# Kernel tuning notes

Measured on AMD Instinct MI355X. Metric: run time of the kernel, lower is better.

The kernel has to match this reference:

```python
import jax, jax.numpy as jnp
import numpy as np

N_NODES = 100000
N_EDGES = 1600000
D_IN = 128
D_OUT = 128


def setup_inputs() -> dict:
    key = jax.random.key(0)
    k1, k2, k3, k4, k5 = jax.random.split(key, 5)
    h = jax.random.normal(k1, (N_NODES, D_IN), dtype=jnp.float32)
    src = jax.random.randint(k2, (N_EDGES,), 0, N_NODES, dtype=jnp.int64)
    dst = jax.random.randint(k3, (N_EDGES,), 0, N_NODES, dtype=jnp.int64)
    # Glorot-ish init for linear weights (PyTorch nn.Linear style: [out, in])
    scale = 1.0 / np.sqrt(D_IN)
    W_self = jax.random.uniform(k4, (D_OUT, D_IN), jnp.float32, -scale, scale)
    W_neigh = jax.random.uniform(k5, (D_OUT, D_IN), jnp.float32, -scale, scale)
    b = jnp.zeros((D_OUT,), dtype=jnp.float32)
    return {"h": h, "src": src, "dst": dst, "W_self": W_self,
            "W_neigh": W_neigh, "b": b}


def reference(h, src, dst, W_self, W_neigh, b):
    n_nodes = h.shape[0]
    # neighbor gather + segment-mean over in-neighbors (DGL fn.copy_u + fn.mean)
    msg = h[src]                                            # [E, D_in]
    neigh_sum = jax.ops.segment_sum(msg, dst, num_segments=n_nodes)
    deg = jax.ops.segment_sum(jnp.ones_like(dst, dtype=h.dtype), dst,
                              num_segments=n_nodes)         # [N]
    h_neigh = neigh_sum / jnp.maximum(deg, 1.0)[:, None]    # mean; 0 for isolated
    # SAGEConv mean: fc_self(h) + fc_neigh(h_neigh) + bias
    out = h @ W_self.T + h_neigh @ W_neigh.T + b
    return out
```

## Files before the change

kernel.cpp:

```cpp
#include <hip/hip_runtime.h>
#include <stdint.h>

#define NN 100000
#define NE 1600000
#define DD 128
#define NTILES ((NN + 127) / 128)
#define NB 512
#define CHUNK (NE / NB)
#define NBUCK ((NN + 255) / 256)
#define BCAP 4608
#define QCAP 1536

typedef __bf16 bf16x8 __attribute__((ext_vector_type(8)));
typedef float f32x4 __attribute__((ext_vector_type(4)));
typedef float f32x2 __attribute__((ext_vector_type(2)));

__device__ __forceinline__ unsigned int f2bf2(float a, float b) {
  union { float f; unsigned u; } x, y;
  x.f = a; y.f = b;
  unsigned ua = x.u + (0x7FFFu + ((x.u >> 16) & 1u));
  unsigned ub = y.u + (0x7FFFu + ((y.u >> 16) & 1u));
  return (ua >> 16) | (ub & 0xFFFF0000u);
}

__global__ __launch_bounds__(256) void zero_kernel(int* __restrict__ gcur) {
  int t = blockIdx.x * 256 + threadIdx.x;
  if (t < NBUCK) gcur[t] = 0;
}

__global__ __launch_bounds__(256) void convert_kernel(
    const float4* __restrict__ hp, uint2* __restrict__ h8,
    uint4* __restrict__ hbf) {
  int t = threadIdx.x, b = blockIdx.x;
  int gid = b * 256 + t;
  float4 a = hp[2 * gid], c = hp[2 * gid + 1];
  int lo = __builtin_amdgcn_cvt_pk_fp8_f32(a.x, a.y, 0, false);
  lo = __builtin_amdgcn_cvt_pk_fp8_f32(a.z, a.w, lo, true);
  int hi = __builtin_amdgcn_cvt_pk_fp8_f32(c.x, c.y, 0, false);
  hi = __builtin_amdgcn_cvt_pk_fp8_f32(c.z, c.w, hi, true);
  h8[gid] = make_uint2((unsigned)lo, (unsigned)hi);

  uint4 q;
  q.x = f2bf2(a.x, a.y);
  q.y = f2bf2(a.z, a.w);
  q.z = f2bf2(c.x, c.y);
  q.w = f2bf2(c.z, c.w);
  int m = t >> 4, c8 = t & 15;
  int rt = b & 7, kc = c8 >> 2, quad = c8 & 3;
  hbf[(size_t)(b >> 3) * 2048 + (((rt << 2) + kc) << 6) + (quad << 4) + m] = q;
}

__global__ __launch_bounds__(256) void coarse_scatter_kernel(
    const int* __restrict__ src, const int* __restrict__ dst,
    int* __restrict__ gcur, unsigned* __restrict__ ebuf) {
  __shared__ int lhp[512];
  __shared__ int lbase[NBUCK];
  __shared__ int lcur[NBUCK];
  __shared__ int gstart[NBUCK];
  __shared__ unsigned sdata[CHUNK];
  __shared__ int sgpos[CHUNK];
  int t = threadIdx.x, b = blockIdx.x;
  lhp[t] = 0;
  lhp[t + 256] = 0;
  __syncthreads();
  int e0 = b * CHUNK;
  for (int e = e0 + t; e < e0 + CHUNK; e += 256)
    atomicAdd(&lhp[dst[e] >> 8], 1);
  __syncthreads();
  int c0 = lhp[t], c1 = lhp[t + 256];
  for (int d = 1; d < 512; d <<= 1) {
    int x0 = (t >= d) ? lhp[t - d] : 0;
    int x1 = ((t + 256) >= d) ? lhp[t + 256 - d] : 0;
    __syncthreads();
    lhp[t] += x0;
    lhp[t + 256] += x1;
    __syncthreads();
  }
  if (t < NBUCK) {
    lbase[t] = lhp[t] - c0;
    lcur[t] = 0;
    gstart[t] = t * BCAP + (c0 ? atomicAdd(&gcur[t], c0) : 0);
  }
  int i2 = t + 256;
  if (i2 < NBUCK) {
    lbase[i2] = lhp[i2] - c1;
    lcur[i2] = 0;
    gstart[i2] = i2 * BCAP + (c1 ? atomicAdd(&gcur[i2], c1) : 0);
  }
  __syncthreads();
  for (int e = e0 + t; e < e0 + CHUNK; e += 256) {
    int d = dst[e], s = src[e];
    int bk = d >> 8;
    int slot = atomicAdd(&lcur[bk], 1);
    int lp = lbase[bk] + slot;
    sdata[lp] = ((unsigned)(d & 255) << 24) | (unsigned)s;
    sgpos[lp] = gstart[bk] + slot;
  }
  __syncthreads();
  for (int j = t; j < CHUNK; j += 256) ebuf[sgpos[j]] = sdata[j];
}

__device__ __forceinline__ void acc16(float* a, uint4 u) {
  f32x2 p;
  p = __builtin_amdgcn_cvt_pk_f32_fp8(u.x, false); a[0] += p.x;  a[1] += p.y;
  p = __builtin_amdgcn_cvt_pk_f32_fp8(u.x, true);  a[2] += p.x;  a[3] += p.y;
  p = __builtin_amdgcn_cvt_pk_f32_fp8(u.y, false); a[4] += p.x;  a[5] += p.y;
  p = __builtin_amdgcn_cvt_pk_f32_fp8(u.y, true);  a[6] += p.x;  a[7] += p.y;
  p = __builtin_amdgcn_cvt_pk_f32_fp8(u.z, false); a[8] += p.x;  a[9] += p.y;
  p = __builtin_amdgcn_cvt_pk_f32_fp8(u.z, true);  a[10] += p.x; a[11] += p.y;
  p = __builtin_amdgcn_cvt_pk_f32_fp8(u.w, false); a[12] += p.x; a[13] += p.y;
  p = __builtin_amdgcn_cvt_pk_f32_fp8(u.w, true);  a[14] += p.x; a[15] += p.y;
}

__global__ __launch_bounds__(256, 4) void gather_bucket_kernel(
    const unsigned* __restrict__ ebuf, const int* __restrict__ gcur,
    const uint4* __restrict__ h8, uint4* __restrict__ hfrag) {
  __shared__ int hist[64], st[64], cur[64];
  __shared__ int ssort[QCAP];
  int t = threadIdx.x, bid = blockIdx.x;
  int g = bid >> 2, qt = bid & 3;
  int base = g * BCAP;
  int cnt = gcur[g];
  int lo = qt * 64;
  if (t < 64) hist[t] = 0;
  __syncthreads();
  for (int j = t; j < cnt; j += 256) {
    int dn = (int)(ebuf[base + j] >> 24) - lo;
    if ((unsigned)dn < 64u) atomicAdd(&hist[dn], 1);
  }
  __syncthreads();
  if (t < 64) st[t] = hist[t];
  __syncthreads();
  for (int d = 1; d < 64; d <<= 1) {
    int x = (t < 64 && t >= d) ? st[t - d] : 0;
    __syncthreads();
    if (t < 64) st[t] += x;
    __syncthreads();
  }
  if (t < 64) {
    int s = st[t] - hist[t];
    st[t] = s;
    cur[t] = s;
  }
  __syncthreads();
  for (int j = t; j < cnt; j += 256) {
    unsigned e = ebuf[base + j];
    int dn = (int)(e >> 24) - lo;
    if ((unsigned)dn < 64u) {
      int pos = atomicAdd(&cur[dn], 1);
      if (pos < QCAP) ssort[pos] = (int)(e & 0x00FFFFFFu);
    }
  }
  __syncthreads();
  int grp = t >> 3, l = t & 7;
  uint4* bp = hfrag + (size_t)(bid >> 1) * 2048;
#pragma unroll 1
  for (int rnd = 0; rnd < 2; rnd++) {
    int li = rnd * 32 + grp;
    int deg = hist[li];
    int j0 = st[li];
    float a[16];
#pragma unroll
    for (int i = 0; i < 16; i++) a[i] = 0.f;
    int jmax = deg & ~3;
    if (jmax > 0) {
      int s0 = ssort[j0], s1 = ssort[j0 + 1], s2 = ssort[j0 + 2], s3 = ssort[j0 + 3];
      uint4 u0 = h8[(size_t)s0 * 8 + l];
      uint4 u1 = h8[(size_t)s1 * 8 + l];
      uint4 u2 = h8[(size_t)s2 * 8 + l];
      uint4 u3 = h8[(size_t)s3 * 8 + l];
      for (int j4 = 4; j4 < jmax; j4 += 4) {
        int t0 = ssort[j0 + j4], t1 = ssort[j0 + j4 + 1];
        int t2 = ssort[j0 + j4 + 2], t3 = ssort[j0 + j4 + 3];
        uint4 v0 = h8[(size_t)t0 * 8 + l];
        uint4 v1 = h8[(size_t)t1 * 8 + l];
        uint4 v2 = h8[(size_t)t2 * 8 + l];
        uint4 v3 = h8[(size_t)t3 * 8 + l];
        acc16(a, u0); acc16(a, u1); acc16(a, u2); acc16(a, u3);
        u0 = v0; u1 = v1; u2 = v2; u3 = v3;
      }
      acc16(a, u0); acc16(a, u1); acc16(a, u2); acc16(a, u3);
    }
    for (int j2 = jmax; j2 < deg; j2++) acc16(a, h8[(size_t)ssort[j0 + j2] * 8 + l]);
    float sc = (deg > 0) ? (1.0f / (float)deg) : 0.0f;
    uint4 r0, r1;
    r0.x = f2bf2(a[0] * sc, a[1] * sc);   r0.y = f2bf2(a[2] * sc, a[3] * sc);
    r0.z = f2bf2(a[4] * sc, a[5] * sc);   r0.w = f2bf2(a[6] * sc, a[7] * sc);
    r1.x = f2bf2(a[8] * sc, a[9] * sc);   r1.y = f2bf2(a[10] * sc, a[11] * sc);
    r1.z = f2bf2(a[12] * sc, a[13] * sc); r1.w = f2bf2(a[14] * sc, a[15] * sc);
    int r = ((qt & 1) << 6) + li;
    int rt = r >> 4, m = r & 15;
    int kc = l >> 1, quad = (l & 1) << 1;
    int slot = (((rt << 2) + kc) << 6) + (quad << 4) + m;
    bp[slot] = r0;
    bp[slot + 16] = r1;
  }
}

__device__ __forceinline__ void stage_w(const float* __restrict__ X,
                                        uint4* buf, int t) {
#pragma unroll
  for (int i = 0; i < 8; i++) {
    int id = t + (i << 8);
    int r = id >> 4;
    int c8 = id & 15;
    const float4* p = (const float4*)(X + (size_t)r * DD + (c8 << 3));
    float4 v0 = p[0], v1 = p[1];
    uint4 q;
    q.x = f2bf2(v0.x, v0.y);
    q.y = f2bf2(v0.z, v0.w);
    q.z = f2bf2(v1.x, v1.y);
    q.w = f2bf2(v1.z, v1.w);
    int rt = r >> 4, m = r & 15, kc = c8 >> 2, quad = c8 & 3;
    buf[(((rt << 2) + kc) << 6) + (quad << 4) + m] = q;
  }
}

__device__ __forceinline__ void compute_reg(const uint4* a, const uint4* sWb,
                                            f32x4 acc[2][8], int lane) {
#pragma unroll
  for (int kc = 0; kc < 4; kc++) {
    bf16x8 bfr[8];
#pragma unroll
    for (int n = 0; n < 8; n++)
      bfr[n] = *(const bf16x8*)&sWb[(((n << 2) + kc) << 6) + lane];
    bf16x8 a0 = *(const bf16x8*)&a[kc];
    bf16x8 a1 = *(const bf16x8*)&a[4 + kc];
#pragma unroll
    for (int n = 0; n < 8; n++) {
      acc[0][n] = __builtin_amdgcn_mfma_f32_16x16x32_bf16(a0, bfr[n], acc[0][n], 0, 0, 0);
      acc[1][n] = __builtin_amdgcn_mfma_f32_16x16x32_bf16(a1, bfr[n], acc[1][n], 0, 0, 0);
    }
  }
}

__global__ __launch_bounds__(256, 4) void gemm_kernel(
    const uint4* __restrict__ hbf, const uint4* __restrict__ hfrag,
    const float* __restrict__ Wself, const float* __restrict__ Wneigh,
    const float* __restrict__ bias, float* __restrict__ out) {
  __shared__ uint4 sW[2048];
  int t = threadIdx.x;
  int wv = t >> 6;
  int lane = t & 63;
  int row0 = blockIdx.x * 128;

  const uint4* fb1 = hbf + (size_t)blockIdx.x * 2048;
  const uint4* fb2 = hfrag + (size_t)blockIdx.x * 2048;
  uint4 a1[8], a2[8];
#pragma unroll
  for (int kc = 0; kc < 4; kc++) {
    int s0 = ((((wv * 2 + 0) << 2) + kc) << 6) + lane;
    int s1 = ((((wv * 2 + 1) << 2) + kc) << 6) + lane;
    a1[kc] = fb1[s0]; a1[4 + kc] = fb1[s1];
    a2[kc] = fb2[s0]; a2[4 + kc] = fb2[s1];
  }

  f32x4 acc[2][8];
#pragma unroll
  for (int i = 0; i < 2; i++)
#pragma unroll
    for (int n = 0; n < 8; n++) acc[i][n] = f32x4{0.f, 0.f, 0.f, 0.f};

  stage_w(Wself, sW, t);
  __syncthreads();
  compute_reg(a1, sW, acc, lane);
  __syncthreads();
  stage_w(Wneigh, sW, t);
  __syncthreads();
  compute_reg(a2, sW, acc, lane);

  int col = lane & 15, rq = lane >> 4;
  float bv[8];
#pragma unroll
  for (int n = 0; n < 8; n++) bv[n] = bias[n * 16 + col];
#pragma unroll
  for (int rt = 0; rt < 2; rt++) {
    int rb = row0 + (wv * 2 + rt) * 16 + rq * 4;
#pragma unroll
    for (int r = 0; r < 4; r++) {
      int row = rb + r;
      if (row < NN) {
        float* op = out + (size_t)row * DD + col;
#pragma unroll
        for (int n = 0; n < 8; n++) op[n * 16] = acc[rt][n][r] + bv[n];
      }
    }
  }
}

extern "C" void kernel_launch(void* const* d_in, const int* in_sizes, int n_in,
                              void* d_out, int out_size, void* d_ws, size_t ws_size,
                              hipStream_t stream) {
  const float* h      = (const float*)d_in[0];
  const int*   src    = (const int*)d_in[1];
  const int*   dst    = (const int*)d_in[2];
  const float* Wself  = (const float*)d_in[3];
  const float* Wneigh = (const float*)d_in[4];
  const float* bias   = (const float*)d_in[5];
  float* out = (float*)d_out;

  char* ws = (char*)d_ws;
  unsigned* h8       = (unsigned*)ws;
  unsigned* hbf      = (unsigned*)(ws + 12800000);
  unsigned* hfrag    = (unsigned*)(ws + 38424576);
  unsigned* ebuf     = (unsigned*)(ws + 64049152);
  int*      gcur     = (int*)(ws + 71256064);

  zero_kernel<<<2, 256, 0, stream>>>(gcur);
  convert_kernel<<<6250, 256, 0, stream>>>((const float4*)h, (uint2*)h8,
                                           (uint4*)hbf);
  coarse_scatter_kernel<<<NB, 256, 0, stream>>>(src, dst, gcur, ebuf);
  gather_bucket_kernel<<<NBUCK * 4, 256, 0, stream>>>(ebuf, gcur,
                                                      (const uint4*)h8,
                                                      (uint4*)hfrag);
  gemm_kernel<<<NTILES, 256, 0, stream>>>((const uint4*)hbf, (const uint4*)hfrag,
                                          Wself, Wneigh, bias, out);
}
```

Baseline: 221.6 us.

## Fuse convert and coarse scatter kernels, pack fp8 accumulation, raise gather occupancy

Merges the h conversion kernel and the edge coarse-scatter kernel into one launch. The first NB blocks also do the bucket scatter after their conversion work, and the rest exit early. This removes one kernel launch and the gap between the two stages. The cost is that every conversion block now reserves the scatter's large shared-memory footprint, which can limit how many blocks fit per CU. The gather kernel also accumulates into f32x2 vectors so packed float adds can be used, and its launch bound hint rises from 4 to 8 blocks to push for higher occupancy, at some register-pressure risk.

```diff
diff --git a/kernel.cpp b/kernel.cpp
--- a/kernel.cpp
+++ b/kernel.cpp
@@ -28,9 +28,17 @@
   if (t < NBUCK) gcur[t] = 0;
 }
 
-__global__ __launch_bounds__(256) void convert_kernel(
+__global__ __launch_bounds__(256) void convert_scatter_kernel(
     const float4* __restrict__ hp, uint2* __restrict__ h8,
-    uint4* __restrict__ hbf) {
+    uint4* __restrict__ hbf, const int* __restrict__ src,
+    const int* __restrict__ dst, int* __restrict__ gcur,
+    unsigned* __restrict__ ebuf) {
+  __shared__ int lhp[512];
+  __shared__ int lbase[NBUCK];
+  __shared__ int lcur[NBUCK];
+  __shared__ int gstart[NBUCK];
+  __shared__ unsigned sdata[CHUNK];
+  __shared__ int sgpos[CHUNK];
   int t = threadIdx.x, b = blockIdx.x;
   int gid = b * 256 + t;
   float4 a = hp[2 * gid], c = hp[2 * gid + 1];
@@ -48,18 +56,9 @@
   int m = t >> 4, c8 = t & 15;
   int rt = b & 7, kc = c8 >> 2, quad = c8 & 3;
   hbf[(size_t)(b >> 3) * 2048 + (((rt << 2) + kc) << 6) + (quad << 4) + m] = q;
-}
-
-__global__ __launch_bounds__(256) void coarse_scatter_kernel(
-    const int* __restrict__ src, const int* __restrict__ dst,
-    int* __restrict__ gcur, unsigned* __restrict__ ebuf) {
-  __shared__ int lhp[512];
-  __shared__ int lbase[NBUCK];
-  __shared__ int lcur[NBUCK];
-  __shared__ int gstart[NBUCK];
-  __shared__ unsigned sdata[CHUNK];
-  __shared__ int sgpos[CHUNK];
-  int t = threadIdx.x, b = blockIdx.x;
+
+  if (b >= NB) return;
+
   lhp[t] = 0;
   lhp[t + 256] = 0;
   __syncthreads();
@@ -100,19 +99,18 @@
   for (int j = t; j < CHUNK; j += 256) ebuf[sgpos[j]] = sdata[j];
 }
 
-__device__ __forceinline__ void acc16(float* a, uint4 u) {
-  f32x2 p;
-  p = __builtin_amdgcn_cvt_pk_f32_fp8(u.x, false); a[0] += p.x;  a[1] += p.y;
-  p = __builtin_amdgcn_cvt_pk_f32_fp8(u.x, true);  a[2] += p.x;  a[3] += p.y;
-  p = __builtin_amdgcn_cvt_pk_f32_fp8(u.y, false); a[4] += p.x;  a[5] += p.y;
-  p = __builtin_amdgcn_cvt_pk_f32_fp8(u.y, true);  a[6] += p.x;  a[7] += p.y;
-  p = __builtin_amdgcn_cvt_pk_f32_fp8(u.z, false); a[8] += p.x;  a[9] += p.y;
-  p = __builtin_amdgcn_cvt_pk_f32_fp8(u.z, true);  a[10] += p.x; a[11] += p.y;
-  p = __builtin_amdgcn_cvt_pk_f32_fp8(u.w, false); a[12] += p.x; a[13] += p.y;
-  p = __builtin_amdgcn_cvt_pk_f32_fp8(u.w, true);  a[14] += p.x; a[15] += p.y;
-}
-
-__global__ __launch_bounds__(256, 4) void gather_bucket_kernel(
+__device__ __forceinline__ void acc16p(f32x2* a, uint4 u) {
+  a[0] += __builtin_amdgcn_cvt_pk_f32_fp8(u.x, false);
+  a[1] += __builtin_amdgcn_cvt_pk_f32_fp8(u.x, true);
+  a[2] += __builtin_amdgcn_cvt_pk_f32_fp8(u.y, false);
+  a[3] += __builtin_amdgcn_cvt_pk_f32_fp8(u.y, true);
+  a[4] += __builtin_amdgcn_cvt_pk_f32_fp8(u.z, false);
+  a[5] += __builtin_amdgcn_cvt_pk_f32_fp8(u.z, true);
+  a[6] += __builtin_amdgcn_cvt_pk_f32_fp8(u.w, false);
+  a[7] += __builtin_amdgcn_cvt_pk_f32_fp8(u.w, true);
+}
+
+__global__ __launch_bounds__(256, 8) void gather_bucket_kernel(
     const unsigned* __restrict__ ebuf, const int* __restrict__ gcur,
     const uint4* __restrict__ h8, uint4* __restrict__ hfrag) {
   __shared__ int hist[64], st[64], cur[64];
@@ -159,9 +157,9 @@
     int li = rnd * 32 + grp;
     int deg = hist[li];
     int j0 = st[li];
-    float a[16];
-#pragma unroll
-    for (int i = 0; i < 16; i++) a[i] = 0.f;
+    f32x2 a[8];
+#pragma unroll
+    for (int i = 0; i < 8; i++) a[i] = f32x2{0.f, 0.f};
     int jmax = deg & ~3;
     if (jmax > 0) {
       int s0 = ssort[j0], s1 = ssort[j0 + 1], s2 = ssort[j0 + 2], s3 = ssort[j0 + 3];
@@ -176,18 +174,21 @@
         uint4 v1 = h8[(size_t)t1 * 8 + l];
         uint4 v2 = h8[(size_t)t2 * 8 + l];
         uint4 v3 = h8[(size_t)t3 * 8 + l];
-        acc16(a, u0); acc16(a, u1); acc16(a, u2); acc16(a, u3);
+        acc16p(a, u0); acc16p(a, u1); acc16p(a, u2); acc16p(a, u3);
         u0 = v0; u1 = v1; u2 = v2; u3 = v3;
       }
-      acc16(a, u0); acc16(a, u1); acc16(a, u2); acc16(a, u3);
+      acc16p(a, u0); acc16p(a, u1); acc16p(a, u2); acc16p(a, u3);
     }
-    for (int j2 = jmax; j2 < deg; j2++) acc16(a, h8[(size_t)ssort[j0 + j2] * 8 + l]);
+    for (int j2 = jmax; j2 < deg; j2++) acc16p(a, h8[(size_t)ssort[j0 + j2] * 8 + l]);
     float sc = (deg > 0) ? (1.0f / (float)deg) : 0.0f;
+    f32x2 s2 = {sc, sc};
+#pragma unroll
+    for (int i = 0; i < 8; i++) a[i] *= s2;
     uint4 r0, r1;
-    r0.x = f2bf2(a[0] * sc, a[1] * sc);   r0.y = f2bf2(a[2] * sc, a[3] * sc);
-    r0.z = f2bf2(a[4] * sc, a[5] * sc);   r0.w = f2bf2(a[6] * sc, a[7] * sc);
-    r1.x = f2bf2(a[8] * sc, a[9] * sc);   r1.y = f2bf2(a[10] * sc, a[11] * sc);
-    r1.z = f2bf2(a[12] * sc, a[13] * sc); r1.w = f2bf2(a[14] * sc, a[15] * sc);
+    r0.x = f2bf2(a[0].x, a[0].y);  r0.y = f2bf2(a[1].x, a[1].y);
+    r0.z = f2bf2(a[2].x, a[2].y);  r0.w = f2bf2(a[3].x, a[3].y);
+    r1.x = f2bf2(a[4].x, a[4].y);  r1.y = f2bf2(a[5].x, a[5].y);
+    r1.z = f2bf2(a[6].x, a[6].y);  r1.w = f2bf2(a[7].x, a[7].y);
     int r = ((qt & 1) << 6) + li;
     int rt = r >> 4, m = r & 15;
     int kc = l >> 1, quad = (l & 1) << 1;
@@ -307,9 +308,9 @@
   int*      gcur     = (int*)(ws + 71256064);
 
   zero_kernel<<<2, 256, 0, stream>>>(gcur);
-  convert_kernel<<<6250, 256, 0, stream>>>((const float4*)h, (uint2*)h8,
-                                           (uint4*)hbf);
-  coarse_scatter_kernel<<<NB, 256, 0, stream>>>(src, dst, gcur, ebuf);
+  convert_scatter_kernel<<<6250, 256, 0, stream>>>((const float4*)h, (uint2*)h8,
+                                                   (uint4*)hbf, src, dst, gcur,
+                                                   ebuf);
   gather_bucket_kernel<<<NBUCK * 4, 256, 0, stream>>>(ebuf, gcur,
                                                       (const uint4*)h8,
                                                       (uint4*)hfrag);
```

New measurement: 203.3 us. 1.09x faster.
